# Optimization experiments

Measured on AMD Instinct MI355X. Metric: run time of the kernel, lower is better.

The kernel has to match this reference:

```python
import jax, jax.numpy as jnp
import numpy as np

C, H, W = 9, 180, 240
B, N = 8, 100000


def setup_inputs() -> dict:
    key = jax.random.key(0)
    ks = jax.random.split(key, 10)
    x = jax.random.randint(ks[0], (B, N), 0, W, dtype=jnp.int32)
    y = jax.random.randint(ks[1], (B, N), 0, H, dtype=jnp.int32)
    p = jax.random.randint(ks[2], (B, N), 0, 2, dtype=jnp.int32)  # polarity already mapped to {0,1}
    t = jax.random.uniform(ks[3], (B, N), dtype=jnp.float32)       # normalized timestamps in [0,1]
    # ValueLayer MLP params: Linear(1,100) -> LeakyReLU(0.1) -> Linear(100,100) -> LeakyReLU(0.1) -> Linear(100,1)
    # stored as [in, out] so application is x @ w + b
    w1 = jax.random.normal(ks[4], (1, 100), dtype=jnp.float32) * 0.5
    b1 = jax.random.normal(ks[5], (100,), dtype=jnp.float32) * 0.1
    w2 = jax.random.normal(ks[6], (100, 100), dtype=jnp.float32) * 0.1
    b2 = jax.random.normal(ks[7], (100,), dtype=jnp.float32) * 0.1
    w3 = jax.random.normal(ks[8], (100, 1), dtype=jnp.float32) * 0.1
    b3 = jax.random.normal(ks[9], (1,), dtype=jnp.float32) * 0.1
    return {"t": t, "w1": w1, "b1": b1, "w2": w2, "b2": b2, "w3": w3, "b3": b3,
            "x": x, "y": y, "p": p}


def _value_layer(ts, w1, b1, w2, b2, w3, b3):
    # ts: [M] -> [M]; tiny 1->100->100->1 MLP with LeakyReLU(0.1)
    h = jax.nn.leaky_relu(ts[:, None] * w1[0] + b1, negative_slope=0.1)  # [M,100]
    h = jax.nn.leaky_relu(h @ w2 + b2, negative_slope=0.1)               # [M,100]
    return (h @ w3)[:, 0] + b3[0]                                        # [M]


def reference(t, w1, b1, w2, b2, w3, b3, x, y, p):
    num_voxels = 2 * C * H * W * B
    b_idx = jnp.arange(B, dtype=jnp.int32)[:, None]  # batch index per event row
    # flat base index: x + W*y + W*H*C*p + W*H*C*2*b
    idx_before = (x + W * y + W * H * C * p + W * H * C * 2 * b_idx).reshape(-1)  # [B*N]
    tf = t.reshape(-1)  # [B*N]
    vox = jnp.zeros((num_voxels,), dtype=tf.dtype)
    for i_bin in range(C):  # small fixed loop over temporal bins
        values = tf * _value_layer(tf - i_bin / (C - 1), w1, b1, w2, b2, w3, b3)
        idx = jnp.clip(idx_before + W * H * i_bin, 0, num_voxels - 1)
        vox = vox.at[idx].add(values)
    vox = vox.reshape(B, 2, C, H, W)
    return jnp.concatenate([vox[:, 0], vox[:, 1]], axis=1)  # [B, 2C, H, W]
```

## Files before the change

kernel.cpp:

```cpp
#include <hip/hip_runtime.h>
#include <hip/hip_bf16.h>

#define Cc   9
#define Hh   180
#define Ww   240
#define Bb   8
#define Nn   100000
#define WH   (Ww * Hh)
#define WHC  (WH * Cc)

#define TSIZE 2048

#define TPB   90
#define LBKT  (2 * TPB)
#define NBKT  (LBKT * Bb)
#define CAP   1024

#define CHUNK 2048
#define CHUNKS_PB 49
#define APPEND_BLOCKS (CHUNKS_PB * Bb)
#define TABLE_BLOCKS  257
#define PREP_BLOCKS   (APPEND_BLOCKS + TABLE_BLOCKS)
#define STG   64

#define SORT_OFF 0
#define TAB_OFF  (NBKT * CAP * 4)
#define CURS_OFF (TAB_OFF + (TSIZE + 1) * 4)
#define WS_NEED  (CURS_OFF + NBKT * 4)

#define NCELL 480

__device__ __forceinline__ float leaky(float v) {
    return v >= 0.0f ? v : 0.1f * v;
}

__global__ __launch_bounds__(256) void prep_kernel(
        const int* __restrict__ ex, const int* __restrict__ ey,
        const int* __restrict__ ep, const float* __restrict__ t,
        const float* __restrict__ w1, const float* __restrict__ b1,
        const float* __restrict__ w2, const float* __restrict__ b2,
        const float* __restrict__ w3, const float* __restrict__ b3,
        int* __restrict__ curs, unsigned* __restrict__ sorted,
        float* __restrict__ tab) {
    __shared__ unsigned buf[LBKT * STG];
    __shared__ int cnt[LBKT];
    __shared__ int bse[LBKT];

    if (blockIdx.x < APPEND_BLOCKS) {
        const int b = blockIdx.x / CHUNKS_PB;
        const int chunk = blockIdx.x % CHUNKS_PB;
        for (int i = threadIdx.x; i < LBKT; i += 256) cnt[i] = 0;
        __syncthreads();

        int* curs_b = curs + b * LBKT;
        unsigned* sorted_b = sorted + (size_t)b * LBKT * CAP;

        const int base_e = chunk * CHUNK + threadIdx.x;
        #pragma unroll
        for (int k = 0; k < 8; ++k) {
            int e = base_e + k * 256;
            if (e < Nn) {
                int gi = b * Nn + e;
                int x = __builtin_nontemporal_load(ex + gi);
                int y = __builtin_nontemporal_load(ey + gi);
                int p = __builtin_nontemporal_load(ep + gi);
                float tf = __builtin_nontemporal_load(t + gi);
                int m = (int)(tf * 32768.0f + 0.5f);
                if (m > 32767) m = 32767;
                unsigned wv = (unsigned)x | ((unsigned)y << 8) |
                              ((unsigned)p << 16) | ((unsigned)m << 17);
                int lb = p * TPB + (y >> 1);
                int pos = atomicAdd(&cnt[lb], 1);
                if (pos < STG) {
                    buf[lb * STG + pos] = wv;
                } else {
                    int gp = atomicAdd(&curs_b[lb], 1);
                    if (gp < CAP) sorted_b[lb * CAP + gp] = wv;
                }
            }
        }
        __syncthreads();
        if (threadIdx.x < LBKT) {
            int c = cnt[threadIdx.x];
            if (c > STG) c = STG;
            cnt[threadIdx.x] = c;
            bse[threadIdx.x] = c ? atomicAdd(&curs_b[threadIdx.x], c) : 0;
        }
        __syncthreads();
        const int wid = threadIdx.x >> 6;
        const int lane = threadIdx.x & 63;
        for (int lb = wid; lb < LBKT; lb += 4) {
            int c = cnt[lb];
            if (lane < c) {
                int gp = bse[lb] + lane;
                if (gp < CAP) sorted_b[lb * CAP + gp] = buf[lb * STG + lane];
            }
        }
    } else {
        float* red = (float*)bse;
        const int tblk = blockIdx.x - APPEND_BLOCKS;
        const int grp = threadIdx.x >> 7;
        const int k = threadIdx.x & 127;
        const int kk = k < 100 ? k : 99;
        for (int rep = 0; rep < 4; ++rep) {
            int point = tblk * 8 + rep * 2 + grp;
            float g = -1.0f + (float)point * (1.0f / (float)(TSIZE / 2));
            float acc = b2[kk];
            #pragma unroll 4
            for (int j = 0; j < 100; ++j) {
                float h1 = leaky(g * w1[j] + b1[j]);
                acc += h1 * w2[j * 100 + kk];
            }
            float part = (k < 100) ? leaky(acc) * w3[k] : 0.0f;
            #pragma unroll
            for (int off = 32; off > 0; off >>= 1)
                part += __shfl_down(part, off, 64);
            __syncthreads();
            if ((threadIdx.x & 63) == 0) red[threadIdx.x >> 6] = part;
            __syncthreads();
            if (k == 0 && point <= TSIZE)
                tab[point] = red[grp * 2] + red[grp * 2 + 1] + b3[0];
        }
    }
}

__global__ __launch_bounds__(256) void accum_kernel(
        const unsigned* __restrict__ sorted, const int* __restrict__ curs,
        const float* __restrict__ tab, float* __restrict__ out) {
    __shared__ float2 stab2[TSIZE + 1];
    __shared__ unsigned evsorted[CAP];
    __shared__ int hist[512];
    __shared__ int wsum[8];

    const int bkt = blockIdx.x;
    const int b2p = bkt / TPB;
    const int ytile = bkt % TPB;
    const int tid = threadIdx.x;
    const int lane = tid & 63;
    const int wid = tid >> 6;

    for (int i = tid; i <= TSIZE; i += 256) {
        float v = tab[i];
        float v1 = (i < TSIZE) ? tab[i + 1] : v;
        stab2[i] = make_float2(v, v1 - v);
    }
    for (int i = tid; i < 512; i += 256) hist[i] = 0;

    int cnt = curs[bkt];
    if (cnt > CAP) cnt = CAP;
    const unsigned* sb = sorted + (size_t)bkt * CAP;
    __syncthreads();

    unsigned wreg[4];
    #pragma unroll
    for (int j = 0; j < 4; ++j) {
        int e = tid + j * 256;
        wreg[j] = 0;
        if (e < cnt) {
            unsigned w = sb[e];
            wreg[j] = w;
            int cell = ((w >> 8) & 1) * Ww + (w & 255);
            atomicAdd(&hist[cell], 1);
        }
    }
    __syncthreads();

    int own[2], incl[2];
    #pragma unroll
    for (int r = 0; r < 2; ++r) {
        int i = r * 256 + tid;
        int x = hist[i];
        own[r] = x;
        #pragma unroll
        for (int d = 1; d < 64; d <<= 1) {
            int y = __shfl_up(x, d, 64);
            if (lane >= d) x += y;
        }
        incl[r] = x;
        if (lane == 63) wsum[r * 4 + wid] = x;
    }
    __syncthreads();
    if (tid == 0) {
        int a = 0;
        #pragma unroll
        for (int s = 0; s < 8; ++s) { int v = wsum[s]; wsum[s] = a; a += v; }
    }
    __syncthreads();
    #pragma unroll
    for (int r = 0; r < 2; ++r) {
        int i = r * 256 + tid;
        hist[i] = wsum[r * 4 + wid] + incl[r] - own[r];
    }
    __syncthreads();

    #pragma unroll
    for (int j = 0; j < 4; ++j) {
        int e = tid + j * 256;
        if (e < cnt) {
            unsigned w = wreg[j];
            int cell = ((w >> 8) & 1) * Ww + (w & 255);
            int pos = atomicAdd(&hist[cell], 1);
            evsorted[pos] = w;
        }
    }
    __syncthreads();

    const int y0 = ytile * 2;
    for (int c = tid; c < NCELL; c += 256) {
        int s = c ? hist[c - 1] : 0;
        int e_end = hist[c];
        float bin[Cc];
        #pragma unroll
        for (int i = 0; i < Cc; ++i) bin[i] = 0.0f;
        for (int e = s; e < e_end; ++e) {
            unsigned w = evsorted[e];
            int m = (int)(w >> 17);
            float tfr = (float)m * (1.0f / 32768.0f);
            int U = m + 32768;
            #pragma unroll
            for (int i = 0; i < Cc; ++i) {
                int Ui = U - i * 4096;
                int iu = Ui >> 5;
                float fr = (float)(Ui & 31) * 0.03125f;
                float2 td = stab2[iu];
                bin[i] += tfr * (td.x + fr * td.y);
            }
        }
        int dy = c / Ww;
        int x = c % Ww;
        #pragma unroll
        for (int i = 0; i < Cc; ++i)
            out[(b2p * Cc + i) * WH + (y0 + dy) * Ww + x] = bin[i];
    }
}

__global__ __launch_bounds__(128) void build_table_kernel(
        const float* __restrict__ w1, const float* __restrict__ b1,
        const float* __restrict__ w2, const float* __restrict__ b2,
        const float* __restrict__ w3, const float* __restrict__ b3,
        float* __restrict__ tab) {
    const int i = blockIdx.x;
    const int k = threadIdx.x;
    const int kk = k < 100 ? k : 99;
    const float g = -1.0f + (2.0f / (float)TSIZE) * (float)i;
    float acc = b2[kk];
    #pragma unroll 4
    for (int j = 0; j < 100; ++j) {
        float h1 = leaky(g * w1[j] + b1[j]);
        acc += h1 * w2[j * 100 + kk];
    }
    float part = 0.0f;
    if (k < 100) part = leaky(acc) * w3[k];
    #pragma unroll
    for (int off = 32; off > 0; off >>= 1) part += __shfl_down(part, off, 64);
    __shared__ float red[2];
    if ((k & 63) == 0) red[k >> 6] = part;
    __syncthreads();
    if (k == 0) tab[i] = red[0] + red[1] + b3[0];
}

__global__ __launch_bounds__(256) void scatter_kernel(
        const float* __restrict__ t,
        const int* __restrict__ ex, const int* __restrict__ ey,
        const int* __restrict__ ep,
        const float* __restrict__ tab,
        float* __restrict__ out) {
    __shared__ float stab[TSIZE + 1];
    for (int i = threadIdx.x; i < TSIZE + 1; i += 256) stab[i] = tab[i];
    __syncthreads();
    const int b = blockIdx.x & 7;
    const int chunk = blockIdx.x >> 3;
    const int e = chunk * 256 + threadIdx.x;
    if (e >= Nn) return;
    const int gi = b * Nn + e;
    const float tf = t[gi];
    const int base = ex[gi] + Ww * ey[gi] + WHC * ep[gi] + 2 * WHC * b;
    #pragma unroll
    for (int i = 0; i < Cc; ++i) {
        float ts = tf - 0.125f * (float)i;
        float u = (ts + 1.0f) * (float)(TSIZE / 2);
        u = fmaxf(u, 0.0f);
        int iu = (int)u;
        if (iu > TSIZE - 1) iu = TSIZE - 1;
        float fr = u - (float)iu;
        float v0 = stab[iu];
        float v1 = stab[iu + 1];
        atomicAdd(out + base + WH * i, tf * (v0 + fr * (v1 - v0)));
    }
}

extern "C" void kernel_launch(void* const* d_in, const int* in_sizes, int n_in,
                              void* d_out, int out_size, void* d_ws, size_t ws_size,
                              hipStream_t stream) {
    const float* t  = (const float*)d_in[0];
    const float* w1 = (const float*)d_in[1];
    const float* b1 = (const float*)d_in[2];
    const float* w2 = (const float*)d_in[3];
    const float* b2 = (const float*)d_in[4];
    const float* w3 = (const float*)d_in[5];
    const float* b3 = (const float*)d_in[6];
    const int*   ex = (const int*)d_in[7];
    const int*   ey = (const int*)d_in[8];
    const int*   ep = (const int*)d_in[9];
    float* out = (float*)d_out;
    char* ws = (char*)d_ws;

    if (ws_size >= (size_t)WS_NEED) {
        unsigned* sorted = (unsigned*)(ws + SORT_OFF);
        float*    tab    = (float*)(ws + TAB_OFF);
        int*      curs   = (int*)(ws + CURS_OFF);

        hipMemsetAsync(curs, 0, NBKT * sizeof(int), stream);
        prep_kernel<<<PREP_BLOCKS, 256, 0, stream>>>(
            ex, ey, ep, t, w1, b1, w2, b2, w3, b3, curs, sorted, tab);
        accum_kernel<<<NBKT, 256, 0, stream>>>(sorted, curs, tab, out);
    } else {
        float* tab = (float*)ws;
        hipMemsetAsync(d_out, 0, (size_t)out_size * sizeof(float), stream);
        build_table_kernel<<<TSIZE + 1, 128, 0, stream>>>(w1, b1, w2, b2, w3, b3, tab);
        const int chunks = (Nn + 255) / 256;
        scatter_kernel<<<chunks * Bb, 256, 0, stream>>>(t, ex, ey, ep, tab, out);
    }
}
```

Before: 123.6 us.

## Fuse prep and accumulate kernels into persistent kernel with grid barrier

Merges the bucketing/table-build kernel and the per-bucket accumulation kernel into one persistent kernel of 256 blocks. The blocks meet at a software grid barrier built on a global atomic counter, then pull buckets dynamically from a shared counter. Each block also builds part of the value table after appending its events. The aim is to remove a kernel launch and the tail gap between kernels. The risks are deadlock if not all 256 blocks are resident at once, fewer blocks for the append phase, and spin-wait cost at the barrier. Output stores become nontemporal.

```diff
diff --git a/kernel.cpp b/kernel.cpp
--- a/kernel.cpp
+++ b/kernel.cpp
@@ -15,222 +15,242 @@
 #define LBKT  (2 * TPB)
 #define NBKT  (LBKT * Bb)
 #define CAP   1024
-
-#define CHUNK 2048
-#define CHUNKS_PB 49
-#define APPEND_BLOCKS (CHUNKS_PB * Bb)
-#define TABLE_BLOCKS  257
-#define PREP_BLOCKS   (APPEND_BLOCKS + TABLE_BLOCKS)
 #define STG   64
+#define NCELL 480
+
+#define GRID  256
+#define EVB   3125
 
 #define SORT_OFF 0
 #define TAB_OFF  (NBKT * CAP * 4)
 #define CURS_OFF (TAB_OFF + (TSIZE + 1) * 4)
-#define WS_NEED  (CURS_OFF + NBKT * 4)
-
-#define NCELL 480
+#define BAR_OFF  (CURS_OFF + NBKT * 4)
+#define WS_NEED  (BAR_OFF + 8)
+
+#define SH_BYTES (LBKT * STG * 4 + 2 * LBKT * 4)
 
 __device__ __forceinline__ float leaky(float v) {
     return v >= 0.0f ? v : 0.1f * v;
 }
 
-__global__ __launch_bounds__(256) void prep_kernel(
+__global__ __launch_bounds__(256) void fused_kernel(
         const int* __restrict__ ex, const int* __restrict__ ey,
         const int* __restrict__ ep, const float* __restrict__ t,
         const float* __restrict__ w1, const float* __restrict__ b1,
         const float* __restrict__ w2, const float* __restrict__ b2,
         const float* __restrict__ w3, const float* __restrict__ b3,
         int* __restrict__ curs, unsigned* __restrict__ sorted,
-        float* __restrict__ tab) {
-    __shared__ unsigned buf[LBKT * STG];
-    __shared__ int cnt[LBKT];
-    __shared__ int bse[LBKT];
-
-    if (blockIdx.x < APPEND_BLOCKS) {
-        const int b = blockIdx.x / CHUNKS_PB;
-        const int chunk = blockIdx.x % CHUNKS_PB;
-        for (int i = threadIdx.x; i < LBKT; i += 256) cnt[i] = 0;
-        __syncthreads();
-
-        int* curs_b = curs + b * LBKT;
-        unsigned* sorted_b = sorted + (size_t)b * LBKT * CAP;
-
-        const int base_e = chunk * CHUNK + threadIdx.x;
-        #pragma unroll
-        for (int k = 0; k < 8; ++k) {
-            int e = base_e + k * 256;
-            if (e < Nn) {
-                int gi = b * Nn + e;
-                int x = __builtin_nontemporal_load(ex + gi);
-                int y = __builtin_nontemporal_load(ey + gi);
-                int p = __builtin_nontemporal_load(ep + gi);
-                float tf = __builtin_nontemporal_load(t + gi);
-                int m = (int)(tf * 32768.0f + 0.5f);
-                if (m > 32767) m = 32767;
-                unsigned wv = (unsigned)x | ((unsigned)y << 8) |
-                              ((unsigned)p << 16) | ((unsigned)m << 17);
-                int lb = p * TPB + (y >> 1);
-                int pos = atomicAdd(&cnt[lb], 1);
-                if (pos < STG) {
-                    buf[lb * STG + pos] = wv;
-                } else {
-                    int gp = atomicAdd(&curs_b[lb], 1);
-                    if (gp < CAP) sorted_b[lb * CAP + gp] = wv;
-                }
-            }
-        }
-        __syncthreads();
-        if (threadIdx.x < LBKT) {
-            int c = cnt[threadIdx.x];
-            if (c > STG) c = STG;
-            cnt[threadIdx.x] = c;
-            bse[threadIdx.x] = c ? atomicAdd(&curs_b[threadIdx.x], c) : 0;
-        }
-        __syncthreads();
-        const int wid = threadIdx.x >> 6;
-        const int lane = threadIdx.x & 63;
-        for (int lb = wid; lb < LBKT; lb += 4) {
-            int c = cnt[lb];
-            if (lane < c) {
-                int gp = bse[lb] + lane;
-                if (gp < CAP) sorted_b[lb * CAP + gp] = buf[lb * STG + lane];
-            }
-        }
-    } else {
-        float* red = (float*)bse;
-        const int tblk = blockIdx.x - APPEND_BLOCKS;
-        const int grp = threadIdx.x >> 7;
-        const int k = threadIdx.x & 127;
-        const int kk = k < 100 ? k : 99;
-        for (int rep = 0; rep < 4; ++rep) {
-            int point = tblk * 8 + rep * 2 + grp;
-            float g = -1.0f + (float)point * (1.0f / (float)(TSIZE / 2));
+        float* __restrict__ tab, int* __restrict__ bar,
+        float* __restrict__ out) {
+    __shared__ __align__(16) char smem[SH_BYTES];
+    __shared__ float red[4];
+    __shared__ int wsum[8];
+    __shared__ int curbkt;
+
+    const int tid = threadIdx.x;
+    const int lane = tid & 63;
+    const int wid = tid >> 6;
+    const int blk = blockIdx.x;
+
+    unsigned* buf = (unsigned*)smem;
+    int* cnt = (int*)(smem + LBKT * STG * 4);
+    int* bse = cnt + LBKT;
+
+    const int b = blk >> 5;
+    const int chunk = blk & 31;
+    for (int i = tid; i < LBKT; i += 256) cnt[i] = 0;
+    __syncthreads();
+
+    int* curs_b = curs + b * LBKT;
+    unsigned* sorted_b = sorted + (size_t)b * LBKT * CAP;
+    const int e0 = chunk * EVB;
+    #pragma unroll
+    for (int k = 0; k < 13; ++k) {
+        int r = k * 256 + tid;
+        if (r < EVB) {
+            int gi = b * Nn + e0 + r;
+            int x = __builtin_nontemporal_load(ex + gi);
+            int y = __builtin_nontemporal_load(ey + gi);
+            int p = __builtin_nontemporal_load(ep + gi);
+            float tf = __builtin_nontemporal_load(t + gi);
+            int m = (int)(tf * 32768.0f + 0.5f);
+            if (m > 32767) m = 32767;
+            unsigned wv = (unsigned)x | ((unsigned)y << 8) |
+                          ((unsigned)p << 16) | ((unsigned)m << 17);
+            int lb = p * TPB + (y >> 1);
+            int pos = atomicAdd(&cnt[lb], 1);
+            if (pos < STG) {
+                buf[lb * STG + pos] = wv;
+            } else {
+                int gp = atomicAdd(&curs_b[lb], 1);
+                if (gp < CAP) sorted_b[lb * CAP + gp] = wv;
+            }
+        }
+    }
+    __syncthreads();
+    if (tid < LBKT) {
+        int c = cnt[tid];
+        if (c > STG) c = STG;
+        cnt[tid] = c;
+        bse[tid] = c ? atomicAdd(&curs_b[tid], c) : 0;
+    }
+    __syncthreads();
+    for (int lb = wid; lb < LBKT; lb += 4) {
+        int c = cnt[lb];
+        if (lane < c) {
+            int gp = bse[lb] + lane;
+            if (gp < CAP) sorted_b[lb * CAP + gp] = buf[lb * STG + lane];
+        }
+    }
+
+    {
+        const int grp = tid >> 7;
+        const int kx = tid & 127;
+        const int kk = kx < 100 ? kx : 99;
+        const int nrep = (blk == 0) ? 5 : 4;
+        for (int rep = 0; rep < nrep; ++rep) {
+            int point = (rep < 4) ? (blk * 8 + rep * 2 + grp) : (2048 + grp);
+            float g = -1.0f + (float)point * (1.0f / 1024.0f);
             float acc = b2[kk];
             #pragma unroll 4
             for (int j = 0; j < 100; ++j) {
                 float h1 = leaky(g * w1[j] + b1[j]);
                 acc += h1 * w2[j * 100 + kk];
             }
-            float part = (k < 100) ? leaky(acc) * w3[k] : 0.0f;
+            float part = (kx < 100) ? leaky(acc) * w3[kx] : 0.0f;
             #pragma unroll
             for (int off = 32; off > 0; off >>= 1)
                 part += __shfl_down(part, off, 64);
             __syncthreads();
-            if ((threadIdx.x & 63) == 0) red[threadIdx.x >> 6] = part;
+            if ((tid & 63) == 0) red[tid >> 6] = part;
             __syncthreads();
-            if (k == 0 && point <= TSIZE)
+            if (kx == 0 && point <= TSIZE)
                 tab[point] = red[grp * 2] + red[grp * 2 + 1] + b3[0];
         }
     }
-}
-
-__global__ __launch_bounds__(256) void accum_kernel(
-        const unsigned* __restrict__ sorted, const int* __restrict__ curs,
-        const float* __restrict__ tab, float* __restrict__ out) {
-    __shared__ float2 stab2[TSIZE + 1];
-    __shared__ unsigned evsorted[CAP];
-    __shared__ int hist[512];
-    __shared__ int wsum[8];
-
-    const int bkt = blockIdx.x;
-    const int b2p = bkt / TPB;
-    const int ytile = bkt % TPB;
-    const int tid = threadIdx.x;
-    const int lane = tid & 63;
-    const int wid = tid >> 6;
+
+    __threadfence();
+    __syncthreads();
+    if (tid == 0) {
+        __hip_atomic_fetch_add(&bar[0], 1, __ATOMIC_ACQ_REL,
+                               __HIP_MEMORY_SCOPE_AGENT);
+        while (__hip_atomic_load(&bar[0], __ATOMIC_ACQUIRE,
+                                 __HIP_MEMORY_SCOPE_AGENT) < GRID) {
+            __builtin_amdgcn_s_sleep(1);
+        }
+    }
+    __syncthreads();
+    __threadfence();
+
+    float2* stab2 = (float2*)smem;
+    unsigned* evsorted = (unsigned*)(smem + (TSIZE + 1) * 8);
+    int* hist = (int*)(smem + (TSIZE + 1) * 8 + CAP * 4);
 
     for (int i = tid; i <= TSIZE; i += 256) {
         float v = tab[i];
         float v1 = (i < TSIZE) ? tab[i + 1] : v;
         stab2[i] = make_float2(v, v1 - v);
     }
-    for (int i = tid; i < 512; i += 256) hist[i] = 0;
-
-    int cnt = curs[bkt];
-    if (cnt > CAP) cnt = CAP;
-    const unsigned* sb = sorted + (size_t)bkt * CAP;
-    __syncthreads();
-
-    unsigned wreg[4];
-    #pragma unroll
-    for (int j = 0; j < 4; ++j) {
-        int e = tid + j * 256;
-        wreg[j] = 0;
-        if (e < cnt) {
-            unsigned w = sb[e];
-            wreg[j] = w;
-            int cell = ((w >> 8) & 1) * Ww + (w & 255);
-            atomicAdd(&hist[cell], 1);
-        }
-    }
-    __syncthreads();
-
-    int own[2], incl[2];
-    #pragma unroll
-    for (int r = 0; r < 2; ++r) {
-        int i = r * 256 + tid;
-        int x = hist[i];
-        own[r] = x;
+
+    while (true) {
+        if (tid == 0)
+            curbkt = __hip_atomic_fetch_add(&bar[1], 1, __ATOMIC_RELAXED,
+                                            __HIP_MEMORY_SCOPE_AGENT);
+        __syncthreads();
+        const int bkt = curbkt;
+        if (bkt >= NBKT) break;
+        const int b2p = bkt / TPB;
+        const int ytile = bkt % TPB;
+
+        for (int i = tid; i < 512; i += 256) hist[i] = 0;
+        int ccnt = curs[bkt];
+        if (ccnt > CAP) ccnt = CAP;
+        const unsigned* sb = sorted + (size_t)bkt * CAP;
+        __syncthreads();
+
+        unsigned wreg[4];
         #pragma unroll
-        for (int d = 1; d < 64; d <<= 1) {
-            int y = __shfl_up(x, d, 64);
-            if (lane >= d) x += y;
-        }
-        incl[r] = x;
-        if (lane == 63) wsum[r * 4 + wid] = x;
-    }
-    __syncthreads();
-    if (tid == 0) {
-        int a = 0;
+        for (int j = 0; j < 4; ++j) {
+            int e = tid + j * 256;
+            wreg[j] = 0;
+            if (e < ccnt) {
+                unsigned w = sb[e];
+                wreg[j] = w;
+                int cell = ((w >> 8) & 1) * Ww + (w & 255);
+                atomicAdd(&hist[cell], 1);
+            }
+        }
+        __syncthreads();
+
+        int own[2], incl[2];
         #pragma unroll
-        for (int s = 0; s < 8; ++s) { int v = wsum[s]; wsum[s] = a; a += v; }
-    }
-    __syncthreads();
-    #pragma unroll
-    for (int r = 0; r < 2; ++r) {
-        int i = r * 256 + tid;
-        hist[i] = wsum[r * 4 + wid] + incl[r] - own[r];
-    }
-    __syncthreads();
-
-    #pragma unroll
-    for (int j = 0; j < 4; ++j) {
-        int e = tid + j * 256;
-        if (e < cnt) {
-            unsigned w = wreg[j];
-            int cell = ((w >> 8) & 1) * Ww + (w & 255);
-            int pos = atomicAdd(&hist[cell], 1);
-            evsorted[pos] = w;
-        }
-    }
-    __syncthreads();
-
-    const int y0 = ytile * 2;
-    for (int c = tid; c < NCELL; c += 256) {
-        int s = c ? hist[c - 1] : 0;
-        int e_end = hist[c];
-        float bin[Cc];
+        for (int r2 = 0; r2 < 2; ++r2) {
+            int i = r2 * 256 + tid;
+            int xv = hist[i];
+            own[r2] = xv;
+            #pragma unroll
+            for (int d = 1; d < 64; d <<= 1) {
+                int yv = __shfl_up(xv, d, 64);
+                if (lane >= d) xv += yv;
+            }
+            incl[r2] = xv;
+            if (lane == 63) wsum[r2 * 4 + wid] = xv;
+        }
+        __syncthreads();
+        if (tid == 0) {
+            int a = 0;
+            #pragma unroll
+            for (int s = 0; s < 8; ++s) { int v = wsum[s]; wsum[s] = a; a += v; }
+        }
+        __syncthreads();
         #pragma unroll
-        for (int i = 0; i < Cc; ++i) bin[i] = 0.0f;
-        for (int e = s; e < e_end; ++e) {
-            unsigned w = evsorted[e];
-            int m = (int)(w >> 17);
-            float tfr = (float)m * (1.0f / 32768.0f);
-            int U = m + 32768;
-            #pragma unroll
-            for (int i = 0; i < Cc; ++i) {
-                int Ui = U - i * 4096;
-                int iu = Ui >> 5;
-                float fr = (float)(Ui & 31) * 0.03125f;
-                float2 td = stab2[iu];
-                bin[i] += tfr * (td.x + fr * td.y);
-            }
-        }
-        int dy = c / Ww;
-        int x = c % Ww;
+        for (int r2 = 0; r2 < 2; ++r2) {
+            int i = r2 * 256 + tid;
+            hist[i] = wsum[r2 * 4 + wid] + incl[r2] - own[r2];
+        }
+        __syncthreads();
+
         #pragma unroll
-        for (int i = 0; i < Cc; ++i)
-            out[(b2p * Cc + i) * WH + (y0 + dy) * Ww + x] = bin[i];
+        for (int j = 0; j < 4; ++j) {
+            int e = tid + j * 256;
+            if (e < ccnt) {
+                unsigned w = wreg[j];
+                int cell = ((w >> 8) & 1) * Ww + (w & 255);
+                int pos = atomicAdd(&hist[cell], 1);
+                evsorted[pos] = w;
+            }
+        }
+        __syncthreads();
+
+        const int y0 = ytile * 2;
+        for (int c = tid; c < NCELL; c += 256) {
+            int s = c ? hist[c - 1] : 0;
+            int eend = hist[c];
+            float bin[Cc];
+            #pragma unroll
+            for (int i = 0; i < Cc; ++i) bin[i] = 0.0f;
+            for (int e = s; e < eend; ++e) {
+                unsigned w = evsorted[e];
+                int m = (int)(w >> 17);
+                float tfr = (float)m * (1.0f / 32768.0f);
+                int U = m + 32768;
+                #pragma unroll
+                for (int i = 0; i < Cc; ++i) {
+                    int Ui = U - i * 4096;
+                    int iu = Ui >> 5;
+                    float fr = (float)(Ui & 31) * 0.03125f;
+                    float2 td = stab2[iu];
+                    bin[i] += tfr * (td.x + fr * td.y);
+                }
+            }
+            int dy = c / Ww;
+            int xq = c % Ww;
+            #pragma unroll
+            for (int i = 0; i < Cc; ++i)
+                __builtin_nontemporal_store(
+                    bin[i], &out[(b2p * Cc + i) * WH + (y0 + dy) * Ww + xq]);
+        }
+        __syncthreads();
     }
 }
 
@@ -309,11 +329,11 @@
         unsigned* sorted = (unsigned*)(ws + SORT_OFF);
         float*    tab    = (float*)(ws + TAB_OFF);
         int*      curs   = (int*)(ws + CURS_OFF);
-
-        hipMemsetAsync(curs, 0, NBKT * sizeof(int), stream);
-        prep_kernel<<<PREP_BLOCKS, 256, 0, stream>>>(
-            ex, ey, ep, t, w1, b1, w2, b2, w3, b3, curs, sorted, tab);
-        accum_kernel<<<NBKT, 256, 0, stream>>>(sorted, curs, tab, out);
+        int*      bar    = (int*)(ws + BAR_OFF);
+
+        hipMemsetAsync(curs, 0, NBKT * sizeof(int) + 8, stream);
+        fused_kernel<<<GRID, 256, 0, stream>>>(
+            ex, ey, ep, t, w1, b1, w2, b2, w3, b3, curs, sorted, tab, bar, out);
     } else {
         float* tab = (float*)ws;
         hipMemsetAsync(d_out, 0, (size_t)out_size * sizeof(float), stream);
```

After: 219.7 us. 77.8% more time.

## Use 4-row buckets, vectorized event loads, one table point per block

Applied to the files above, without the earlier changes.

Each bucket now covers four image rows instead of two, which halves the bucket count and doubles capacity, cell count and staging size. Event loads in the append phase become int4/float4 vector loads. The MLP table build now computes one pair of points per block, with the first-layer activations cached in shared memory and four independent accumulators. Output writes use nontemporal stores. The aim is lower per-bucket overhead and better load efficiency, at the cost of fewer accumulation blocks (720 vs 1440) and more shared memory per block.

```diff
diff --git a/kernel.cpp b/kernel.cpp
--- a/kernel.cpp
+++ b/kernel.cpp
@@ -11,24 +11,23 @@
 
 #define TSIZE 2048
 
-#define TPB   90
+#define TPB   45
 #define LBKT  (2 * TPB)
 #define NBKT  (LBKT * Bb)
-#define CAP   1024
+#define CAP   2048
+#define STG   96
+#define NCELL 960
 
 #define CHUNK 2048
 #define CHUNKS_PB 49
 #define APPEND_BLOCKS (CHUNKS_PB * Bb)
-#define TABLE_BLOCKS  257
+#define TABLE_BLOCKS  1025
 #define PREP_BLOCKS   (APPEND_BLOCKS + TABLE_BLOCKS)
-#define STG   64
 
 #define SORT_OFF 0
 #define TAB_OFF  (NBKT * CAP * 4)
 #define CURS_OFF (TAB_OFF + (TSIZE + 1) * 4)
 #define WS_NEED  (CURS_OFF + NBKT * 4)
-
-#define NCELL 480
 
 __device__ __forceinline__ float leaky(float v) {
     return v >= 0.0f ? v : 0.1f * v;
@@ -45,31 +44,56 @@
     __shared__ unsigned buf[LBKT * STG];
     __shared__ int cnt[LBKT];
     __shared__ int bse[LBKT];
+    __shared__ float h1s[2][100];
+    __shared__ float red[4];
+
+    const int tid = threadIdx.x;
+    const int lane = tid & 63;
+    const int wid = tid >> 6;
 
     if (blockIdx.x < APPEND_BLOCKS) {
         const int b = blockIdx.x / CHUNKS_PB;
         const int chunk = blockIdx.x % CHUNKS_PB;
-        for (int i = threadIdx.x; i < LBKT; i += 256) cnt[i] = 0;
+        for (int i = tid; i < LBKT; i += 256) cnt[i] = 0;
         __syncthreads();
 
         int* curs_b = curs + b * LBKT;
         unsigned* sorted_b = sorted + (size_t)b * LBKT * CAP;
-
-        const int base_e = chunk * CHUNK + threadIdx.x;
-        #pragma unroll
-        for (int k = 0; k < 8; ++k) {
-            int e = base_e + k * 256;
-            if (e < Nn) {
-                int gi = b * Nn + e;
-                int x = __builtin_nontemporal_load(ex + gi);
-                int y = __builtin_nontemporal_load(ey + gi);
-                int p = __builtin_nontemporal_load(ep + gi);
-                float tf = __builtin_nontemporal_load(t + gi);
-                int m = (int)(tf * 32768.0f + 0.5f);
+        const int e0 = chunk * CHUNK;
+
+        #pragma unroll
+        for (int k = 0; k < 2; ++k) {
+            const int e_ = e0 + k * 1024 + tid * 4;
+            int xs[4], ys[4], ps[4];
+            float tfs[4];
+            int nv = 0;
+            if (e_ + 3 < Nn) {
+                const int gi = b * Nn + e_;
+                int4 xv = *(const int4*)(ex + gi);
+                int4 yv = *(const int4*)(ey + gi);
+                int4 pv = *(const int4*)(ep + gi);
+                float4 tv = *(const float4*)(t + gi);
+                xs[0] = xv.x; xs[1] = xv.y; xs[2] = xv.z; xs[3] = xv.w;
+                ys[0] = yv.x; ys[1] = yv.y; ys[2] = yv.z; ys[3] = yv.w;
+                ps[0] = pv.x; ps[1] = pv.y; ps[2] = pv.z; ps[3] = pv.w;
+                tfs[0] = tv.x; tfs[1] = tv.y; tfs[2] = tv.z; tfs[3] = tv.w;
+                nv = 4;
+            } else {
+                for (int q = 0; q < 4; ++q) {
+                    if (e_ + q < Nn) {
+                        const int gi = b * Nn + e_ + q;
+                        xs[nv] = ex[gi]; ys[nv] = ey[gi];
+                        ps[nv] = ep[gi]; tfs[nv] = t[gi];
+                        ++nv;
+                    }
+                }
+            }
+            for (int q = 0; q < nv; ++q) {
+                int m = (int)(tfs[q] * 32768.0f + 0.5f);
                 if (m > 32767) m = 32767;
-                unsigned wv = (unsigned)x | ((unsigned)y << 8) |
-                              ((unsigned)p << 16) | ((unsigned)m << 17);
-                int lb = p * TPB + (y >> 1);
+                unsigned wv = (unsigned)xs[q] | ((unsigned)ys[q] << 8) |
+                              ((unsigned)ps[q] << 16) | ((unsigned)m << 17);
+                int lb = ps[q] * TPB + (ys[q] >> 2);
                 int pos = atomicAdd(&cnt[lb], 1);
                 if (pos < STG) {
                     buf[lb * STG + pos] = wv;
@@ -80,47 +104,48 @@
             }
         }
         __syncthreads();
-        if (threadIdx.x < LBKT) {
-            int c = cnt[threadIdx.x];
+        if (tid < LBKT) {
+            int c = cnt[tid];
             if (c > STG) c = STG;
-            cnt[threadIdx.x] = c;
-            bse[threadIdx.x] = c ? atomicAdd(&curs_b[threadIdx.x], c) : 0;
-        }
-        __syncthreads();
-        const int wid = threadIdx.x >> 6;
-        const int lane = threadIdx.x & 63;
+            cnt[tid] = c;
+            bse[tid] = c ? atomicAdd(&curs_b[tid], c) : 0;
+        }
+        __syncthreads();
         for (int lb = wid; lb < LBKT; lb += 4) {
             int c = cnt[lb];
-            if (lane < c) {
-                int gp = bse[lb] + lane;
-                if (gp < CAP) sorted_b[lb * CAP + gp] = buf[lb * STG + lane];
+            for (int o = lane; o < c; o += 64) {
+                int gp = bse[lb] + o;
+                if (gp < CAP) sorted_b[lb * CAP + gp] = buf[lb * STG + o];
             }
         }
     } else {
-        float* red = (float*)bse;
-        const int tblk = blockIdx.x - APPEND_BLOCKS;
-        const int grp = threadIdx.x >> 7;
-        const int k = threadIdx.x & 127;
-        const int kk = k < 100 ? k : 99;
-        for (int rep = 0; rep < 4; ++rep) {
-            int point = tblk * 8 + rep * 2 + grp;
-            float g = -1.0f + (float)point * (1.0f / (float)(TSIZE / 2));
-            float acc = b2[kk];
-            #pragma unroll 4
-            for (int j = 0; j < 100; ++j) {
-                float h1 = leaky(g * w1[j] + b1[j]);
-                acc += h1 * w2[j * 100 + kk];
-            }
-            float part = (k < 100) ? leaky(acc) * w3[k] : 0.0f;
-            #pragma unroll
-            for (int off = 32; off > 0; off >>= 1)
-                part += __shfl_down(part, off, 64);
-            __syncthreads();
-            if ((threadIdx.x & 63) == 0) red[threadIdx.x >> 6] = part;
-            __syncthreads();
-            if (k == 0 && point <= TSIZE)
-                tab[point] = red[grp * 2] + red[grp * 2 + 1] + b3[0];
-        }
+        const int tb = blockIdx.x - APPEND_BLOCKS;
+        const int grp = tid >> 7;
+        const int kx = tid & 127;
+        const int kk = kx < 100 ? kx : 99;
+        const int point = tb * 2 + grp;
+        const float g = -1.0f + (float)point * (1.0f / 1024.0f);
+
+        if (kx < 100) h1s[grp][kx] = leaky(g * w1[kx] + b1[kx]);
+        __syncthreads();
+
+        float a0 = 0.f, a1 = 0.f, a2 = 0.f, a3 = 0.f;
+        #pragma unroll 5
+        for (int j = 0; j < 100; j += 4) {
+            a0 += h1s[grp][j]     * w2[j * 100 + kk];
+            a1 += h1s[grp][j + 1] * w2[(j + 1) * 100 + kk];
+            a2 += h1s[grp][j + 2] * w2[(j + 2) * 100 + kk];
+            a3 += h1s[grp][j + 3] * w2[(j + 3) * 100 + kk];
+        }
+        float acc = b2[kk] + ((a0 + a1) + (a2 + a3));
+        float part = (kx < 100) ? leaky(acc) * w3[kx] : 0.0f;
+        #pragma unroll
+        for (int off = 32; off > 0; off >>= 1)
+            part += __shfl_down(part, off, 64);
+        if (lane == 0) red[wid] = part;
+        __syncthreads();
+        if (kx == 0 && point <= TSIZE)
+            tab[point] = red[grp * 2] + red[grp * 2 + 1] + b3[0];
     }
 }
 
@@ -129,8 +154,8 @@
         const float* __restrict__ tab, float* __restrict__ out) {
     __shared__ float2 stab2[TSIZE + 1];
     __shared__ unsigned evsorted[CAP];
-    __shared__ int hist[512];
-    __shared__ int wsum[8];
+    __shared__ int hist[1024];
+    __shared__ int wsum[16];
 
     const int bkt = blockIdx.x;
     const int b2p = bkt / TPB;
@@ -144,75 +169,75 @@
         float v1 = (i < TSIZE) ? tab[i + 1] : v;
         stab2[i] = make_float2(v, v1 - v);
     }
-    for (int i = tid; i < 512; i += 256) hist[i] = 0;
-
-    int cnt = curs[bkt];
-    if (cnt > CAP) cnt = CAP;
+    for (int i = tid; i < 1024; i += 256) hist[i] = 0;
+
+    int ccnt = curs[bkt];
+    if (ccnt > CAP) ccnt = CAP;
     const unsigned* sb = sorted + (size_t)bkt * CAP;
     __syncthreads();
 
-    unsigned wreg[4];
-    #pragma unroll
-    for (int j = 0; j < 4; ++j) {
+    unsigned wreg[8];
+    #pragma unroll
+    for (int j = 0; j < 8; ++j) {
         int e = tid + j * 256;
         wreg[j] = 0;
-        if (e < cnt) {
+        if (e < ccnt) {
             unsigned w = sb[e];
             wreg[j] = w;
-            int cell = ((w >> 8) & 1) * Ww + (w & 255);
+            int cell = ((w >> 8) & 3) * Ww + (w & 255);
             atomicAdd(&hist[cell], 1);
         }
     }
     __syncthreads();
 
-    int own[2], incl[2];
-    #pragma unroll
-    for (int r = 0; r < 2; ++r) {
+    int own[4], incl[4];
+    #pragma unroll
+    for (int r = 0; r < 4; ++r) {
         int i = r * 256 + tid;
-        int x = hist[i];
-        own[r] = x;
+        int xv = hist[i];
+        own[r] = xv;
         #pragma unroll
         for (int d = 1; d < 64; d <<= 1) {
-            int y = __shfl_up(x, d, 64);
-            if (lane >= d) x += y;
-        }
-        incl[r] = x;
-        if (lane == 63) wsum[r * 4 + wid] = x;
+            int yv = __shfl_up(xv, d, 64);
+            if (lane >= d) xv += yv;
+        }
+        incl[r] = xv;
+        if (lane == 63) wsum[r * 4 + wid] = xv;
     }
     __syncthreads();
     if (tid == 0) {
         int a = 0;
         #pragma unroll
-        for (int s = 0; s < 8; ++s) { int v = wsum[s]; wsum[s] = a; a += v; }
-    }
-    __syncthreads();
-    #pragma unroll
-    for (int r = 0; r < 2; ++r) {
+        for (int s = 0; s < 16; ++s) { int v = wsum[s]; wsum[s] = a; a += v; }
+    }
+    __syncthreads();
+    #pragma unroll
+    for (int r = 0; r < 4; ++r) {
         int i = r * 256 + tid;
         hist[i] = wsum[r * 4 + wid] + incl[r] - own[r];
     }
     __syncthreads();
 
     #pragma unroll
-    for (int j = 0; j < 4; ++j) {
+    for (int j = 0; j < 8; ++j) {
         int e = tid + j * 256;
-        if (e < cnt) {
+        if (e < ccnt) {
             unsigned w = wreg[j];
-            int cell = ((w >> 8) & 1) * Ww + (w & 255);
+            int cell = ((w >> 8) & 3) * Ww + (w & 255);
             int pos = atomicAdd(&hist[cell], 1);
             evsorted[pos] = w;
         }
     }
     __syncthreads();
 
-    const int y0 = ytile * 2;
+    const int y0 = ytile * 4;
     for (int c = tid; c < NCELL; c += 256) {
         int s = c ? hist[c - 1] : 0;
-        int e_end = hist[c];
+        int eend = hist[c];
         float bin[Cc];
         #pragma unroll
         for (int i = 0; i < Cc; ++i) bin[i] = 0.0f;
-        for (int e = s; e < e_end; ++e) {
+        for (int e = s; e < eend; ++e) {
             unsigned w = evsorted[e];
             int m = (int)(w >> 17);
             float tfr = (float)m * (1.0f / 32768.0f);
@@ -227,10 +252,11 @@
             }
         }
         int dy = c / Ww;
-        int x = c % Ww;
+        int xq = c % Ww;
         #pragma unroll
         for (int i = 0; i < Cc; ++i)
-            out[(b2p * Cc + i) * WH + (y0 + dy) * Ww + x] = bin[i];
+            __builtin_nontemporal_store(
+                bin[i], &out[(b2p * Cc + i) * WH + (y0 + dy) * Ww + xq]);
     }
 }
 
```

Result: faster. 111.7 us (-9.6%).
